# Performance work log

Measured on AMD Instinct MI355X. Metric: run time of the kernel, lower is better.

Reference implementation:

```python
import jax, jax.numpy as jnp
import numpy as np

B, S, HID = 1, 2048, 4096
NH, NKV, HD = 32, 8, 128
GROUPS = NH // NKV
ROPE_THETA = 10000.0


def rotate_half(x):
    x1, x2 = jnp.split(x, 2, axis=-1)
    return jnp.concatenate([-x2, x1], axis=-1)


def rope_cos_sin(position_ids, head_dim, dtype):
    # inv_freq: [hd/2]; position_ids: [B, S]
    inv_freq = 1.0 / (ROPE_THETA ** (jnp.arange(0, head_dim, 2, dtype=jnp.float32) / head_dim))
    freqs = position_ids.astype(jnp.float32)[..., None] * inv_freq  # [B, S, hd/2]
    emb = jnp.concatenate([freqs, freqs], axis=-1)                  # [B, S, hd]
    return jnp.cos(emb).astype(dtype), jnp.sin(emb).astype(dtype)


def apply_rope(x, cos, sin):
    # x: [B, H, S, hd]; cos/sin: [B, S, hd] -> broadcast over heads
    return x * cos[:, None] + rotate_half(x) * sin[:, None]


def setup_inputs() -> dict:
    key = jax.random.key(0)
    ks = jax.random.split(key, 5)
    scale = 0.02
    return {
        "hidden_states": jax.random.normal(ks[0], (B, S, HID), dtype=jnp.float32),
        "wq": jax.random.normal(ks[1], (HID, NH * HD), dtype=jnp.float32) * scale,
        "wk": jax.random.normal(ks[2], (HID, NKV * HD), dtype=jnp.float32) * scale,
        "wv": jax.random.normal(ks[3], (HID, NKV * HD), dtype=jnp.float32) * scale,
        "wo": jax.random.normal(ks[4], (NH * HD, HID), dtype=jnp.float32) * scale,
        "position_ids": jnp.arange(S, dtype=jnp.int32)[None, :],
    }


def reference(hidden_states, wq, wk, wv, wo, position_ids):
    bsz, q_len, _ = hidden_states.shape
    # projections (nn.Linear, bias=False)
    q = (hidden_states @ wq).reshape(bsz, q_len, NH, HD).transpose(0, 2, 1, 3)   # [B,NH,S,hd]
    k = (hidden_states @ wk).reshape(bsz, q_len, NKV, HD).transpose(0, 2, 1, 3)  # [B,NKV,S,hd]
    v = (hidden_states @ wv).reshape(bsz, q_len, NKV, HD).transpose(0, 2, 1, 3)
    # RoPE applied to Q and K at global positions (prefill: no past cache)
    cos, sin = rope_cos_sin(position_ids, HD, q.dtype)
    q = apply_rope(q, cos, sin)
    k = apply_rope(k, cos, sin)
    # GQA: expand KV heads to query heads
    k_full = jnp.repeat(k, GROUPS, axis=1)  # [B,NH,S,hd]
    v_full = jnp.repeat(v, GROUPS, axis=1)
    # prefill flash attention == causal SDPA
    logits = jnp.einsum('bhqd,bhkd->bhqk', q, k_full) / jnp.sqrt(jnp.asarray(HD, q.dtype))
    causal = jnp.tril(jnp.ones((q_len, q_len), dtype=bool))
    neg = jnp.asarray(jnp.finfo(q.dtype).min, q.dtype)
    logits = jnp.where(causal[None, None], logits, neg)
    probs = jax.nn.softmax(logits, axis=-1)                     # [B,NH,S,S]
    attn = jnp.einsum('bhqk,bhkd->bhqd', probs, v_full)          # [B,NH,S,hd]
    attn_output = attn.transpose(0, 2, 1, 3).reshape(bsz, q_len, NH * HD) @ wo
    # chunked prefill eviction scores: causal attention probs accumulated over
    # all queries, aggregated per KV head group -> [B, NKV, kv_len]
    accumulated_scores = probs.sum(axis=2).reshape(bsz, NKV, GROUPS, q_len).sum(axis=2)
    return attn_output, accumulated_scores
```

## Files before the change

### kernel.cpp

```cpp
#include <hip/hip_runtime.h>
#include <hip/hip_bf16.h>
#include <cstdint>
#include <cstddef>

#define S_LEN 2048
#define HID_DIM 4096
#define NH 32
#define NKV 8
#define HD 128
#define LOG2E 1.4426950408889634f
#define SCALE 0.08838834764831845f

typedef __attribute__((ext_vector_type(8))) short bf16x8;
typedef __attribute__((ext_vector_type(4))) float f32x4;
typedef __attribute__((ext_vector_type(16))) float f32x16;
typedef __attribute__((ext_vector_type(4))) short short4v;
typedef __attribute__((ext_vector_type(4))) unsigned u32x4;

__device__ __forceinline__ short f2bf(float f) {
  union { float f; unsigned u; } v; v.f = f;
  return (short)((v.u + 0x7fffu + ((v.u >> 16) & 1u)) >> 16);
}
__device__ __forceinline__ float bf2f(short s) {
  union { unsigned u; float f; } v; v.u = ((unsigned)(unsigned short)s) << 16;
  return v.f;
}
__device__ __forceinline__ unsigned cvt_pk_bf16(float lo, float hi) {
  unsigned r;
  asm("v_cvt_pk_bf16_f32 %0, %1, %2" : "=v"(r) : "v"(lo), "v"(hi));
  return r;
}
__device__ __forceinline__ void gld_lds16(const void* g, void* l) {
  __builtin_amdgcn_global_load_lds((const __attribute__((address_space(1))) unsigned*)g,
                                   (__attribute__((address_space(3))) unsigned*)l, 16, 0, 0);
}

#define WAITVM4() asm volatile("s_waitcnt vmcnt(4)" ::: "memory")
#define WAITVM0() asm volatile("s_waitcnt vmcnt(0)" ::: "memory")

__global__ void cvt_kernel(const float* __restrict__ in, short* __restrict__ out, int n) {
  int i = (blockIdx.x * 256 + threadIdx.x) * 4;
  if (i < n) {
    float4 f = *(const float4*)(in + i);
    short4v o = { f2bf(f.x), f2bf(f.y), f2bf(f.z), f2bf(f.w) };
    *(short4v*)(out + i) = o;
  }
}

__global__ void tconv_kernel(const float* __restrict__ in, short* __restrict__ out, int R, int C) {
  __shared__ float tile[32][33];
  int tr = blockIdx.y * 32, tc = blockIdx.x * 32;
  int tx = threadIdx.x & 31, ty = threadIdx.x >> 5;
#pragma unroll
  for (int i = 0; i < 32; i += 8)
    tile[ty + i][tx] = in[(size_t)(tr + ty + i) * C + tc + tx];
  __syncthreads();
#pragma unroll
  for (int i = 0; i < 32; i += 8)
    out[(size_t)(tc + ty + i) * R + tr + tx] = f2bf(tile[tx][ty + i]);
}

template<int MODE>
__global__ __launch_bounds__(256, 4) void gemm_bt_kernel(
    const short* __restrict__ A, const short* __restrict__ Bt,
    void* __restrict__ Cout, int M, int N, int K, int rchunk, int cchunk)
{
  __shared__ short As[2][128 * 32];
  __shared__ short Bs[2][128 * 32];
  const int tid = threadIdx.x;
  const int lane = tid & 63;
  const int w = tid >> 6;
  const int wm = w >> 1, wn = w & 1;
  const int xcd = blockIdx.x & 7;
  const int local = blockIdx.x >> 3;
  const int by = (xcd >> 2) * rchunk + (local % rchunk);
  const int bx = (xcd & 3) * cchunk + (local / rchunk);
  const int m0 = by * 128, n0 = bx * 128;

  auto stage = [&](int bb, int k0) {
#pragma unroll
    for (int rep = 0; rep < 2; rep++) {
      int c = rep * 256 + tid;
      int row = c >> 2, slot = c & 3;
      int gs = slot ^ (row & 3);
      gld_lds16(A + (size_t)(m0 + row) * K + k0 + gs * 8, &As[bb][c * 8]);
      gld_lds16(Bt + (size_t)(n0 + row) * K + k0 + gs * 8, &Bs[bb][c * 8]);
    }
  };

  f32x4 acc[4][4];
#pragma unroll
  for (int i = 0; i < 4; i++)
#pragma unroll
    for (int j = 0; j < 4; j++) acc[i][j] = (f32x4){0.f, 0.f, 0.f, 0.f};

  const int NT = K >> 5;
  stage(0, 0);
  for (int kt = 0; kt < NT; kt++) {
    const int b = kt & 1;
    if (kt + 1 < NT) { stage(b ^ 1, (kt + 1) << 5); WAITVM4(); }
    else             { WAITVM0(); }
    __builtin_amdgcn_s_barrier();

    bf16x8 af[4], bf[4];
#pragma unroll
    for (int ms = 0; ms < 4; ms++) {
      int row = wm * 64 + ms * 16 + (lane & 15);
      af[ms] = *(const bf16x8*)(&As[b][row * 32 + (((lane >> 4) ^ (row & 3)) << 3)]);
    }
#pragma unroll
    for (int ns = 0; ns < 4; ns++) {
      int row = wn * 64 + ns * 16 + (lane & 15);
      bf[ns] = *(const bf16x8*)(&Bs[b][row * 32 + (((lane >> 4) ^ (row & 3)) << 3)]);
    }
#pragma unroll
    for (int ms = 0; ms < 4; ms++)
#pragma unroll
      for (int ns = 0; ns < 4; ns++)
        acc[ms][ns] = __builtin_amdgcn_mfma_f32_16x16x32_bf16(af[ms], bf[ns], acc[ms][ns], 0, 0, 0);

    __builtin_amdgcn_s_barrier();
  }

#pragma unroll
  for (int ms = 0; ms < 4; ms++) {
    int mb = m0 + wm * 64 + ms * 16 + ((lane >> 4) << 2);
#pragma unroll
    for (int ns = 0; ns < 4; ns++) {
      int n = n0 + wn * 64 + ns * 16 + (lane & 15);
      if (MODE == 3) {
        short* o = (short*)Cout;
        if (n < NH * HD) {
          int head = n >> 7, d = n & 127;
#pragma unroll
          for (int r = 0; r < 4; r++)
            o[((size_t)head * M + (mb + r)) * HD + d] = f2bf(acc[ms][ns][r]);
        } else if (n < (NH + NKV) * HD) {
          int head = (n - NH * HD) >> 7, d = n & 127;
          short* ok = o + (size_t)NH * S_LEN * HD;
#pragma unroll
          for (int r = 0; r < 4; r++)
            ok[((size_t)head * M + (mb + r)) * HD + d] = f2bf(acc[ms][ns][r]);
        } else {
          int head = (n - (NH + NKV) * HD) >> 7, d = n & 127;
          short* ov = o + (size_t)(NH + NKV) * S_LEN * HD;
          short4v pk;
#pragma unroll
          for (int r = 0; r < 4; r++) pk[r] = f2bf(acc[ms][ns][r]);
          *(short4v*)(ov + ((size_t)head * HD + d) * M + mb) = pk;
        }
      } else {
        float* o = (float*)Cout;
#pragma unroll
        for (int r = 0; r < 4; r++)
          o[(size_t)(mb + r) * N + n] = acc[ms][ns][r];
      }
    }
  }
}

__global__ void rope_kernel(short* __restrict__ q, short* __restrict__ k,
                            const int* __restrict__ pos_ids) {
  const int s = blockIdx.x;
  const int hh = blockIdx.y * 4 + threadIdx.y;
  const int d = threadIdx.x;
  const float pos = (float)pos_ids[s];
  const float inv = __expf(-(float)d * 0.14391157f);
  float sn, c;
  __sincosf(pos * inv, &sn, &c);
  short* base = (hh < NH) ? (q + ((size_t)hh * S_LEN + s) * HD)
                          : (k + ((size_t)(hh - NH) * S_LEN + s) * HD);
  float x1 = bf2f(base[d]), x2 = bf2f(base[d + 64]);
  base[d] = f2bf(x1 * c - x2 * sn);
  base[d + 64] = f2bf(x2 * c + x1 * sn);
}

__global__ __launch_bounds__(256, 3) void attn_kernel(
    const short* __restrict__ Qr, const short* __restrict__ Kr, const short* __restrict__ Vt,
    short* __restrict__ attn_out, float* __restrict__ scores)
{
  __shared__ short Ks[2][64 * 128];
  __shared__ short Vs[128 * 64];
  __shared__ float lbuf[128];

  const int tid = threadIdx.x;
  const int lane = tid & 63;
  const int w = tid >> 6;
  const int r = w & 1;
  const int kh = w >> 1;
  const int h2 = lane >> 5;
  const int l31 = lane & 31;
  const int xcd = blockIdx.x & 7;
  const int j = blockIdx.x >> 3;
  const int h = xcd * 4 + (j & 3);
  const int qt = 31 - (j >> 2);
  const int kvh = xcd;
  const float CS = SCALE * LOG2E;

  const short* KrB = Kr + (size_t)kvh * S_LEN * HD;
  const short* VtB = Vt + (size_t)kvh * HD * S_LEN;

  const int nt = qt + 1;
  const int qbase = qt * 64 + r * 32;
  const int qglob = qbase + l31;

  float* obuf = (float*)Ks;

  auto stageK = [&](int bb, int t) {
    const int kb2 = t * 64;
#pragma unroll
    for (int rep = 0; rep < 4; rep++) {
      int c = rep * 256 + tid;
      int x = c >> 4, slot = c & 15;
      int key = (x & 0x33) | ((x & 4) << 1) | ((x & 8) >> 1);
      int gs = slot ^ (x & 7);
      gld_lds16(KrB + (size_t)(kb2 + key) * HD + gs * 8, &Ks[bb][c * 8]);
    }
  };
  auto stageV = [&](int t) {
    const int kb2 = t * 64;
#pragma unroll
    for (int rep = 0; rep < 4; rep++) {
      int c = rep * 256 + tid;
      int d = c >> 3, slot = c & 7;
      int gs = slot ^ (d & 7);
      gld_lds16(VtB + (size_t)d * S_LEN + kb2 + gs * 8, &Vs[c * 8]);
    }
  };

  bf16x8 qf[8];
  {
    const short* qrow = Qr + ((size_t)h * S_LEN + qglob) * HD + h2 * 8;
#pragma unroll
    for (int kc = 0; kc < 8; kc++) qf[kc] = *(const bf16x8*)(qrow + kc * 16);
  }

  f32x16 oacc[4];
#pragma unroll
  for (int i = 0; i < 4; i++) oacc[i] = (f32x16)(0.f);
  float lsum = 0.f;

  stageK(0, 0);
  for (int t = 0; t < nt; t++) {
    const int b = t & 1;
    const int kb = t * 64;
    WAITVM0();
    __builtin_amdgcn_s_barrier();

    stageV(t);
    if (t + 1 < nt) stageK(b ^ 1, t + 1);

    f32x16 sf = (f32x16)(0.f);
    const int x = kh * 32 + l31;
    __builtin_amdgcn_s_setprio(1);
#pragma unroll
    for (int kc = 0; kc < 8; kc++) {
      bf16x8 kf = *(const bf16x8*)(&Ks[b][x * 128 + (((kc * 2 + h2) ^ (x & 7)) << 3)]);
      sf = __builtin_amdgcn_mfma_f32_32x32x16_bf16(kf, qf[kc], sf, 0, 0, 0);
    }
    __builtin_amdgcn_s_setprio(0);

    float pv16[16];
    const bool diag = (kb + 63 > qbase);
#pragma unroll
    for (int a = 0; a < 4; a++)
#pragma unroll
      for (int cc = 0; cc < 4; cc++) {
        float pv = exp2f(sf[a * 4 + cc] * CS);
        if (diag) {
          int key = kb + kh * 32 + (a >> 1) * 16 + h2 * 8 + (a & 1) * 4 + cc;
          if (key > qglob) pv = 0.f;
        }
        pv16[a * 4 + cc] = pv;
        lsum += pv;
      }

    bf16x8 pa[2];
#pragma unroll
    for (int s = 0; s < 2; s++) {
      u32x4 pw;
      pw[0] = cvt_pk_bf16(pv16[8 * s + 0], pv16[8 * s + 1]);
      pw[1] = cvt_pk_bf16(pv16[8 * s + 2], pv16[8 * s + 3]);
      pw[2] = cvt_pk_bf16(pv16[8 * s + 4], pv16[8 * s + 5]);
      pw[3] = cvt_pk_bf16(pv16[8 * s + 6], pv16[8 * s + 7]);
      pa[s] = __builtin_bit_cast(bf16x8, pw);
    }

    if (t + 1 < nt) WAITVM4();
    else           WAITVM0();
    __builtin_amdgcn_s_barrier();

    __builtin_amdgcn_s_setprio(1);
#pragma unroll
    for (int s = 0; s < 2; s++) {
      const int g = kh * 2 + s;
#pragma unroll
      for (int db = 0; db < 4; db++) {
        int d = db * 32 + l31;
        bf16x8 vf = *(const bf16x8*)(&Vs[d * 64 + (((g * 2 + h2) ^ (d & 7)) << 3)]);
        oacc[db] = __builtin_amdgcn_mfma_f32_32x32x16_bf16(pa[s], vf, oacc[db], 0, 0, 0);
      }
    }
    __builtin_amdgcn_s_setprio(0);
  }

  __builtin_amdgcn_s_barrier();

  lsum += __shfl_xor(lsum, 32);
  if (kh == 0) {
#pragma unroll
    for (int db = 0; db < 4; db++)
#pragma unroll
      for (int r16 = 0; r16 < 16; r16++) {
        int crow = (r16 & 3) + 8 * (r16 >> 2) + 4 * h2;
        obuf[(r * 32 + crow) * 128 + db * 32 + l31] = oacc[db][r16];
      }
    if (lane < 32) lbuf[r * 32 + l31] = lsum;
  }
  __builtin_amdgcn_s_barrier();

  if (kh == 1) {
    float ltot = lsum + lbuf[r * 32 + l31];
    float rlv = 1.f / ltot;
    float rl16[16];
#pragma unroll
    for (int r16 = 0; r16 < 16; r16++)
      rl16[r16] = __shfl(rlv, (r16 & 3) + 8 * (r16 >> 2) + 4 * h2);
#pragma unroll
    for (int db = 0; db < 4; db++) {
      int d = db * 32 + l31;
#pragma unroll
      for (int r16 = 0; r16 < 16; r16++) {
        int crow = (r16 & 3) + 8 * (r16 >> 2) + 4 * h2;
        float o = oacc[db][r16] + obuf[(r * 32 + crow) * 128 + d];
        attn_out[(size_t)(qbase + crow) * HID_DIM + h * HD + d] = f2bf(o * rl16[r16]);
      }
    }
    if (lane < 32) lbuf[64 + r * 32 + l31] = rlv;
  }
  __builtin_amdgcn_s_barrier();

  float rlv = lbuf[64 + r * 32 + l31];
  float rl16[16];
#pragma unroll
  for (int r16 = 0; r16 < 16; r16++)
    rl16[r16] = __shfl(rlv, (r16 & 3) + 8 * (r16 >> 2) + 4 * h2);

  float* sc = scores + (size_t)kvh * S_LEN;
  for (int t = kh; t < nt; t += 2) {
    const int kb = t * 64;
    f32x16 sg[2];
    sg[0] = (f32x16)(0.f); sg[1] = (f32x16)(0.f);
    __builtin_amdgcn_s_setprio(1);
#pragma unroll
    for (int kc = 0; kc < 8; kc++)
#pragma unroll
      for (int bl = 0; bl < 2; bl++) {
        bf16x8 kf = *(const bf16x8*)(KrB + (size_t)(kb + bl * 32 + l31) * HD + kc * 16 + h2 * 8);
        sg[bl] = __builtin_amdgcn_mfma_f32_32x32x16_bf16(qf[kc], kf, sg[bl], 0, 0, 0);
      }
    __builtin_amdgcn_s_setprio(0);

    const bool diag = (kb + 63 > qbase);
#pragma unroll
    for (int bl = 0; bl < 2; bl++) {
      int key = kb + bl * 32 + l31;
      float sum = 0.f;
#pragma unroll
      for (int r16 = 0; r16 < 16; r16++) {
        float pv = exp2f(sg[bl][r16] * CS) * rl16[r16];
        if (diag && key > qbase + (r16 & 3) + 8 * (r16 >> 2) + 4 * h2) pv = 0.f;
        sum += pv;
      }
      sum += __shfl_xor(sum, 32);
      if (lane < 32) atomicAdd(&sc[key], sum);
    }
  }
}

extern "C" void kernel_launch(void* const* d_in, const int* in_sizes, int n_in,
                              void* d_out, int out_size, void* d_ws, size_t ws_size,
                              hipStream_t stream) {
  const float* hs = (const float*)d_in[0];
  const float* wq = (const float*)d_in[1];
  const float* wk = (const float*)d_in[2];
  const float* wv = (const float*)d_in[3];
  const float* wo = (const float*)d_in[4];
  const int* pos = (const int*)d_in[5];
  float* out = (float*)d_out;

  char* ws = (char*)d_ws;
  const size_t off_hs   = 0;
  const size_t off_wqT  = off_hs   + (size_t)S_LEN * HID_DIM * 2;
  const size_t off_wkT  = off_wqT  + (size_t)HID_DIM * HID_DIM * 2;
  const size_t off_wvT  = off_wkT  + (size_t)1024 * HID_DIM * 2;
  const size_t off_woT  = off_wvT  + (size_t)1024 * HID_DIM * 2;
  const size_t off_Qr   = off_woT  + (size_t)HID_DIM * HID_DIM * 2;
  const size_t off_Kr   = off_Qr   + (size_t)NH * S_LEN * HD * 2;
  const size_t off_Vt   = off_Kr   + (size_t)NKV * S_LEN * HD * 2;
  const size_t off_attn = off_Vt   + (size_t)NKV * HD * S_LEN * 2;

  short* hsb  = (short*)(ws + off_hs);
  short* wqT  = (short*)(ws + off_wqT);
  short* wkT  = (short*)(ws + off_wkT);
  short* wvT  = (short*)(ws + off_wvT);
  short* woT  = (short*)(ws + off_woT);
  short* Qr   = (short*)(ws + off_Qr);
  short* Kr   = (short*)(ws + off_Kr);
  short* Vt   = (short*)(ws + off_Vt);
  short* attb = (short*)(ws + off_attn);

  cvt_kernel<<<dim3((S_LEN * HID_DIM) / 1024), 256, 0, stream>>>(hs, hsb, S_LEN * HID_DIM);
  tconv_kernel<<<dim3(128, 128), 256, 0, stream>>>(wq, wqT, HID_DIM, HID_DIM);
  tconv_kernel<<<dim3(32, 128), 256, 0, stream>>>(wk, wkT, HID_DIM, 1024);
  tconv_kernel<<<dim3(32, 128), 256, 0, stream>>>(wv, wvT, HID_DIM, 1024);
  tconv_kernel<<<dim3(128, 128), 256, 0, stream>>>(wo, woT, HID_DIM, HID_DIM);

  gemm_bt_kernel<3><<<768, 256, 0, stream>>>(hsb, wqT, Qr, S_LEN, 6144, HID_DIM, 8, 12);

  rope_kernel<<<dim3(S_LEN, 10), dim3(64, 4), 0, stream>>>(Qr, Kr, pos);

  hipMemsetAsync(out + (size_t)S_LEN * HID_DIM, 0, (size_t)NKV * S_LEN * sizeof(float), stream);
  attn_kernel<<<1024, 256, 0, stream>>>(Qr, Kr, Vt, attb, out + (size_t)S_LEN * HID_DIM);

  gemm_bt_kernel<2><<<512, 256, 0, stream>>>(attb, woT, out, S_LEN, HID_DIM, HID_DIM, 8, 8);
}
```

Measured before the change: 399.1 us.

## Move eviction-score pass out of attention into blocks fused with output projection

The attention kernel no longer recomputes QK^T to build the accumulated eviction scores. It now writes the per-row reciprocal softmax denominators to a workspace buffer. A new kernel launches the 512 output-projection GEMM tiles together with 512 extra blocks that recompute the scores from Q, K and those denominators. This shortens the critical path of the attention kernel and lets the score pass overlap with the GEMM. The cost is an extra global round trip for the denominators and contention between the two kinds of block for compute units.

```diff
diff --git a/kernel.cpp b/kernel.cpp
--- a/kernel.cpp
+++ b/kernel.cpp
@@ -177,11 +177,11 @@
 
 __global__ __launch_bounds__(256, 3) void attn_kernel(
     const short* __restrict__ Qr, const short* __restrict__ Kr, const short* __restrict__ Vt,
-    short* __restrict__ attn_out, float* __restrict__ scores)
+    short* __restrict__ attn_out, float* __restrict__ rlw)
 {
   __shared__ short Ks[2][64 * 128];
   __shared__ short Vs[128 * 64];
-  __shared__ float lbuf[128];
+  __shared__ float lbuf[64];
 
   const int tid = threadIdx.x;
   const int lane = tid & 63;
@@ -336,44 +336,142 @@
         attn_out[(size_t)(qbase + crow) * HID_DIM + h * HD + d] = f2bf(o * rl16[r16]);
       }
     }
-    if (lane < 32) lbuf[64 + r * 32 + l31] = rlv;
-  }
-  __builtin_amdgcn_s_barrier();
-
-  float rlv = lbuf[64 + r * 32 + l31];
-  float rl16[16];
-#pragma unroll
-  for (int r16 = 0; r16 < 16; r16++)
-    rl16[r16] = __shfl(rlv, (r16 & 3) + 8 * (r16 >> 2) + 4 * h2);
-
-  float* sc = scores + (size_t)kvh * S_LEN;
-  for (int t = kh; t < nt; t += 2) {
-    const int kb = t * 64;
-    f32x16 sg[2];
-    sg[0] = (f32x16)(0.f); sg[1] = (f32x16)(0.f);
-    __builtin_amdgcn_s_setprio(1);
-#pragma unroll
-    for (int kc = 0; kc < 8; kc++)
+    if (lane < 32) rlw[(size_t)h * S_LEN + qbase + l31] = rlv;
+  }
+}
+
+__global__ __launch_bounds__(256, 4) void oproj_fused_kernel(
+    const short* __restrict__ A, const short* __restrict__ Bt, float* __restrict__ Cout,
+    const short* __restrict__ Qr, const short* __restrict__ Kr,
+    const float* __restrict__ rlw, float* __restrict__ scores)
+{
+  __shared__ short As[2][128 * 32];
+  __shared__ short Bs[2][128 * 32];
+  const int tid = threadIdx.x;
+  const int lane = tid & 63;
+  const float CS = SCALE * LOG2E;
+
+  if (blockIdx.x < 512) {
+    const int w = tid >> 6;
+    const int wm = w >> 1, wn = w & 1;
+    const int xcd = blockIdx.x & 7;
+    const int local = blockIdx.x >> 3;
+    const int by = (xcd >> 2) * 8 + (local % 8);
+    const int bx = (xcd & 3) * 8 + (local / 8);
+    const int m0 = by * 128, n0 = bx * 128;
+    const int M = S_LEN, N = HID_DIM, K = HID_DIM;
+
+    auto stage = [&](int bb, int k0) {
+#pragma unroll
+      for (int rep = 0; rep < 2; rep++) {
+        int c = rep * 256 + tid;
+        int row = c >> 2, slot = c & 3;
+        int gs = slot ^ (row & 3);
+        gld_lds16(A + (size_t)(m0 + row) * K + k0 + gs * 8, &As[bb][c * 8]);
+        gld_lds16(Bt + (size_t)(n0 + row) * K + k0 + gs * 8, &Bs[bb][c * 8]);
+      }
+    };
+
+    f32x4 acc[4][4];
+#pragma unroll
+    for (int i = 0; i < 4; i++)
+#pragma unroll
+      for (int jj = 0; jj < 4; jj++) acc[i][jj] = (f32x4){0.f, 0.f, 0.f, 0.f};
+
+    const int NT = K >> 5;
+    stage(0, 0);
+    for (int kt = 0; kt < NT; kt++) {
+      const int b = kt & 1;
+      if (kt + 1 < NT) { stage(b ^ 1, (kt + 1) << 5); WAITVM4(); }
+      else             { WAITVM0(); }
+      __builtin_amdgcn_s_barrier();
+
+      bf16x8 af[4], bf[4];
+#pragma unroll
+      for (int ms = 0; ms < 4; ms++) {
+        int row = wm * 64 + ms * 16 + (lane & 15);
+        af[ms] = *(const bf16x8*)(&As[b][row * 32 + (((lane >> 4) ^ (row & 3)) << 3)]);
+      }
+#pragma unroll
+      for (int ns = 0; ns < 4; ns++) {
+        int row = wn * 64 + ns * 16 + (lane & 15);
+        bf[ns] = *(const bf16x8*)(&Bs[b][row * 32 + (((lane >> 4) ^ (row & 3)) << 3)]);
+      }
+#pragma unroll
+      for (int ms = 0; ms < 4; ms++)
+#pragma unroll
+        for (int ns = 0; ns < 4; ns++)
+          acc[ms][ns] = __builtin_amdgcn_mfma_f32_16x16x32_bf16(af[ms], bf[ns], acc[ms][ns], 0, 0, 0);
+
+      __builtin_amdgcn_s_barrier();
+    }
+
+#pragma unroll
+    for (int ms = 0; ms < 4; ms++) {
+      int mb = m0 + wm * 64 + ms * 16 + ((lane >> 4) << 2);
+#pragma unroll
+      for (int ns = 0; ns < 4; ns++) {
+        int n = n0 + wn * 64 + ns * 16 + (lane & 15);
+#pragma unroll
+        for (int r = 0; r < 4; r++)
+          Cout[(size_t)(mb + r) * N + n] = acc[ms][ns][r];
+      }
+    }
+  } else {
+    const int cb = blockIdx.x - 512;
+    const int xcd = cb & 7;
+    const int j = cb >> 3;
+    const int h = xcd * 4 + (j & 3);
+    const int qt = 15 - (j >> 2);
+    const int kvh = xcd;
+    const int w = tid >> 6;
+    const int h2 = lane >> 5;
+    const int l31 = lane & 31;
+    const int qbase = qt * 128 + w * 32;
+
+    const short* KrB = Kr + (size_t)kvh * S_LEN * HD;
+
+    bf16x8 qf[8];
+    {
+      const short* qrow = Qr + ((size_t)h * S_LEN + qbase + l31) * HD + h2 * 8;
+#pragma unroll
+      for (int kc = 0; kc < 8; kc++) qf[kc] = *(const bf16x8*)(qrow + kc * 16);
+    }
+    float rl16[16];
+#pragma unroll
+    for (int r16 = 0; r16 < 16; r16++)
+      rl16[r16] = rlw[(size_t)h * S_LEN + qbase + (r16 & 3) + 8 * (r16 >> 2) + 4 * h2];
+
+    float* sc = scores + (size_t)kvh * S_LEN;
+    const int ntw = (qbase + 31) / 64 + 1;
+    for (int t = 0; t < ntw; t++) {
+      const int kb = t * 64;
+      f32x16 sg[2];
+      sg[0] = (f32x16)(0.f); sg[1] = (f32x16)(0.f);
+      __builtin_amdgcn_s_setprio(1);
+#pragma unroll
+      for (int kc = 0; kc < 8; kc++)
+#pragma unroll
+        for (int bl = 0; bl < 2; bl++) {
+          bf16x8 kf = *(const bf16x8*)(KrB + (size_t)(kb + bl * 32 + l31) * HD + kc * 16 + h2 * 8);
+          sg[bl] = __builtin_amdgcn_mfma_f32_32x32x16_bf16(qf[kc], kf, sg[bl], 0, 0, 0);
+        }
+      __builtin_amdgcn_s_setprio(0);
+
+      const bool diag = (kb + 63 > qbase);
 #pragma unroll
       for (int bl = 0; bl < 2; bl++) {
-        bf16x8 kf = *(const bf16x8*)(KrB + (size_t)(kb + bl * 32 + l31) * HD + kc * 16 + h2 * 8);
-        sg[bl] = __builtin_amdgcn_mfma_f32_32x32x16_bf16(qf[kc], kf, sg[bl], 0, 0, 0);
-      }
-    __builtin_amdgcn_s_setprio(0);
-
-    const bool diag = (kb + 63 > qbase);
-#pragma unroll
-    for (int bl = 0; bl < 2; bl++) {
-      int key = kb + bl * 32 + l31;
-      float sum = 0.f;
-#pragma unroll
-      for (int r16 = 0; r16 < 16; r16++) {
-        float pv = exp2f(sg[bl][r16] * CS) * rl16[r16];
-        if (diag && key > qbase + (r16 & 3) + 8 * (r16 >> 2) + 4 * h2) pv = 0.f;
-        sum += pv;
-      }
-      sum += __shfl_xor(sum, 32);
-      if (lane < 32) atomicAdd(&sc[key], sum);
+        int key = kb + bl * 32 + l31;
+        float sum = 0.f;
+#pragma unroll
+        for (int r16 = 0; r16 < 16; r16++) {
+          float pv = exp2f(sg[bl][r16] * CS) * rl16[r16];
+          if (diag && key > qbase + (r16 & 3) + 8 * (r16 >> 2) + 4 * h2) pv = 0.f;
+          sum += pv;
+        }
+        sum += __shfl_xor(sum, 32);
+        if (lane < 32) atomicAdd(&sc[key], sum);
+      }
     }
   }
 }
@@ -399,6 +497,7 @@
   const size_t off_Kr   = off_Qr   + (size_t)NH * S_LEN * HD * 2;
   const size_t off_Vt   = off_Kr   + (size_t)NKV * S_LEN * HD * 2;
   const size_t off_attn = off_Vt   + (size_t)NKV * HD * S_LEN * 2;
+  const size_t off_rlw  = off_attn + (size_t)S_LEN * HID_DIM * 2;
 
   short* hsb  = (short*)(ws + off_hs);
   short* wqT  = (short*)(ws + off_wqT);
@@ -409,6 +508,7 @@
   short* Kr   = (short*)(ws + off_Kr);
   short* Vt   = (short*)(ws + off_Vt);
   short* attb = (short*)(ws + off_attn);
+  float* rlw  = (float*)(ws + off_rlw);
 
   cvt_kernel<<<dim3((S_LEN * HID_DIM) / 1024), 256, 0, stream>>>(hs, hsb, S_LEN * HID_DIM);
   tconv_kernel<<<dim3(128, 128), 256, 0, stream>>>(wq, wqT, HID_DIM, HID_DIM);
@@ -421,7 +521,8 @@
   rope_kernel<<<dim3(S_LEN, 10), dim3(64, 4), 0, stream>>>(Qr, Kr, pos);
 
   hipMemsetAsync(out + (size_t)S_LEN * HID_DIM, 0, (size_t)NKV * S_LEN * sizeof(float), stream);
-  attn_kernel<<<1024, 256, 0, stream>>>(Qr, Kr, Vt, attb, out + (size_t)S_LEN * HID_DIM);
-
-  gemm_bt_kernel<2><<<512, 256, 0, stream>>>(attb, woT, out, S_LEN, HID_DIM, HID_DIM, 8, 8);
-}
+  attn_kernel<<<1024, 256, 0, stream>>>(Qr, Kr, Vt, attb, rlw);
+
+  oproj_fused_kernel<<<1024, 256, 0, stream>>>(attb, woT, out, Qr, Kr, rlw,
+                                               out + (size_t)S_LEN * HID_DIM);
+}
```

After: 399.3 us. No clear change (+0.0%).
